# Performance work log

Hardware: AMD Instinct MI355X
Metric: run time of the kernel (lower is better)

The kernel has to match this reference:

```python
import jax, jax.numpy as jnp
import numpy as np

NUM_HEADS = 16
HEAD_DIM = 64  # hidden = 1024


def setup_inputs() -> dict:
    key = jax.random.key(0)
    k1, k2, k3 = jax.random.split(key, 3)
    B, S, Hd = 4, 4096, NUM_HEADS * HEAD_DIM
    x = jax.random.normal(k1, (B, S, Hd), dtype=jnp.float32)
    # xavier-uniform-ish scaling for the dense kernels
    Wqkv = jax.random.normal(k2, (Hd, 3 * Hd), dtype=jnp.float32) * (2.0 / (Hd + 3 * Hd)) ** 0.5
    bqkv = jnp.zeros((3 * Hd,), dtype=jnp.float32)
    Wout = jax.random.normal(k3, (Hd, Hd), dtype=jnp.float32) * (1.0 / Hd) ** 0.5
    bout = jnp.zeros((Hd,), dtype=jnp.float32)
    return {"x": x, "Wqkv": Wqkv, "bqkv": bqkv, "Wout": Wout, "bout": bout}


def reference(x, Wqkv, bqkv, Wout, bout):
    B, S, _ = x.shape
    H, D = NUM_HEADS, HEAD_DIM
    qkv = jnp.einsum('bsc,cf->bsf', x, Wqkv) + bqkv  # [B,S,3*H*D]
    q, k, v = jnp.split(qkv, 3, axis=-1)
    # source transposes to [B,H,S,D] before calling flax dot_product_attention_weights,
    # which interprets dims as [..., q_len=H, num_heads=S, depth=D]  (shape bug, kept faithfully)
    q = q.reshape(B, S, H, D).transpose(0, 2, 1, 3)  # [B,H,S,D]
    k = k.reshape(B, S, H, D).transpose(0, 2, 1, 3)
    v = v.reshape(B, S, H, D).transpose(0, 2, 1, 3)
    scale = D ** -0.5
    # flax: einsum('...qhd,...khd->...hqk') -> weights [B, S, H, H]
    logits = jnp.einsum('bqhd,bkhd->bhqk', q * scale, k)
    attn = jax.nn.softmax(logits, axis=-1)  # softmax over key-head axis
    # source: einsum('bhqk,bkhd->bqhd', weights, v) -> [B, H, S, D]
    out = jnp.einsum('bhqk,bkhd->bqhd', attn, v)
    out = out.transpose(0, 2, 1, 3).reshape(B, S, H * D)  # [B,S,hidden]
    return jnp.einsum('bsc,cf->bsf', out, Wout) + bout
```

## Files before the change

kernel.cpp:

```cpp
#include <hip/hip_runtime.h>
#include <hip/hip_bf16.h>

using bf16 = __hip_bfloat16;
typedef __bf16 bf16x8_t __attribute__((ext_vector_type(8)));
typedef float f32x4_t __attribute__((ext_vector_type(4)));

__device__ __forceinline__ void gl16(bf16* l, const bf16* g) {
  __builtin_amdgcn_global_load_lds(
      (const __attribute__((address_space(1))) unsigned int*)g,
      (__attribute__((address_space(3))) unsigned int*)l, 16, 0, 0);
}

#define BARRIER() do { asm volatile("" ::: "memory"); __builtin_amdgcn_s_barrier(); asm volatile("" ::: "memory"); } while (0)
#define WAITVM(N) asm volatile("s_waitcnt vmcnt(" #N ")" ::: "memory")
#define SCHED0() __builtin_amdgcn_sched_barrier(0)

__global__ __launch_bounds__(256) void cvt_f32_bf16(const float* __restrict__ in,
                                                    bf16* __restrict__ out, int n4) {
  int i = blockIdx.x * 256 + threadIdx.x;
  if (i >= n4) return;
  float4 v = ((const float4*)in)[i];
  union { ushort4 u; bf16 b[4]; } o;
  o.b[0] = __float2bfloat16(v.x);
  o.b[1] = __float2bfloat16(v.y);
  o.b[2] = __float2bfloat16(v.z);
  o.b[3] = __float2bfloat16(v.w);
  ((ushort4*)out)[i] = o.u;
}

__global__ __launch_bounds__(256) void transpose_cvt(const float* __restrict__ in,
                                                     bf16* __restrict__ out, int R, int C) {
  __shared__ float t[32][33];
  int bx = blockIdx.x * 32, by = blockIdx.y * 32;
  int tx = threadIdx.x & 31, ty = threadIdx.x >> 5;
#pragma unroll
  for (int r = 0; r < 32; r += 8)
    t[ty + r][tx] = in[(size_t)(by + ty + r) * C + bx + tx];
  __syncthreads();
#pragma unroll
  for (int r = 0; r < 32; r += 8)
    out[(size_t)(bx + ty + r) * R + by + tx] = __float2bfloat16(t[tx][ty + r]);
}


__device__ __forceinline__ void readA(const bf16* lb, int half, int wr, int lr, int lg, int exr,
                                      bf16x8_t (&af)[4][2]) {
  const bf16* ab = lb + half * 8192;
#pragma unroll
  for (int mi = 0; mi < 4; ++mi) {
    int R = wr * 64 + mi * 16 + lr;
    af[mi][0] = *(const bf16x8_t*)(ab + R * 64 + ((lg * 8) ^ exr));
    af[mi][1] = *(const bf16x8_t*)(ab + R * 64 + ((32 + lg * 8) ^ exr));
  }
}
__device__ __forceinline__ void readB(const bf16* lb, int half, int wc, int lr, int lg, int exr,
                                      bf16x8_t (&bfr)[2][2]) {
  const bf16* bb = lb + (2 + half) * 8192;
#pragma unroll
  for (int ni = 0; ni < 2; ++ni) {
    int R = wc * 32 + ni * 16 + lr;
    bfr[ni][0] = *(const bf16x8_t*)(bb + R * 64 + ((lg * 8) ^ exr));
    bfr[ni][1] = *(const bf16x8_t*)(bb + R * 64 + ((32 + lg * 8) ^ exr));
  }
}

template <int MH, int NH>
__device__ __forceinline__ void mfma16(bf16x8_t (&af)[4][2], bf16x8_t (&bfr)[2][2],
                                       f32x4_t (&acc)[8][4]) {
  __builtin_amdgcn_s_setprio(1);
#pragma unroll
  for (int mi = 0; mi < 4; ++mi)
#pragma unroll
    for (int ni = 0; ni < 2; ++ni) {
      f32x4_t& a = acc[MH * 4 + mi][NH * 2 + ni];
      a = __builtin_amdgcn_mfma_f32_16x16x32_bf16(af[mi][0], bfr[ni][0], a, 0, 0, 0);
      a = __builtin_amdgcn_mfma_f32_16x16x32_bf16(af[mi][1], bfr[ni][1], a, 0, 0, 0);
    }
  __builtin_amdgcn_s_setprio(0);
}

template <int OUT_BF16, int NWGX>
__global__ __launch_bounds__(512, 2) void gemm256p(const bf16* __restrict__ A,
                                                   const bf16* __restrict__ Bt,
                                                   const float* __restrict__ bias,
                                                   void* __restrict__ Cv) {
  constexpr int K = 1024;
  constexpr int N = NWGX * 256;
  constexpr int TT = NWGX / 4;
  constexpr int G = TT * 16;
  constexpr int CPX = NWGX * 8;

  __shared__ __align__(16) bf16 lds[65536];
  const int tid = threadIdx.x;
  const int bx = blockIdx.x;

  const int wid = tid >> 6, lane = tid & 63;
  const int wr = wid >> 2, wc = wid & 3;
  const int lr = lane & 15, lg = lane >> 4;
  const int exr = (lr & 7) << 3;

  const int srow = tid >> 3;
  const int colg = ((((tid & 7) * 16) ^ ((srow & 7) << 4)) >> 1);
  const int browc0 = (srow >> 5) * 64 + (srow & 31);

  auto tileMN = [&](int tt, int& m0, int& n0) {
    int orig = bx + (tt << 8);
    int swz = (orig & 7) * CPX + (orig >> 3);
    m0 = (swz / NWGX) * 256;
    n0 = (swz % NWGX) * 256;
  };

  auto stageA = [&](int g, int h) {
    if (g >= G) return;
    int m0, n0; tileMN(g >> 4, m0, n0);
    const bf16* g0 = A + (size_t)(m0 + h * 64 + srow) * K + (g & 15) * 64 + colg;
    bf16* l = lds + (g & 1) * 32768 + h * 8192 + tid * 8;
    gl16(l, g0); gl16(l + 4096, g0 + (size_t)128 * K);
  };
  auto stageB = [&](int g, int h) {
    if (g >= G) return;
    int m0, n0; tileMN(g >> 4, m0, n0);
    const bf16* g0 = Bt + (size_t)(n0 + browc0 + h * 32) * K + (g & 15) * 64 + colg;
    bf16* l = lds + (g & 1) * 32768 + (2 + h) * 8192 + tid * 8;
    gl16(l, g0); gl16(l + 4096, g0 + (size_t)128 * K);
  };

  f32x4_t acc[8][4] = {};
  bf16x8_t af1[4][2], af2[4][2], b0[2][2], b1[2][2];

  stageA(0, 0); stageB(0, 0); stageA(0, 1); stageB(0, 1);
  stageA(1, 0); stageB(1, 0);
  WAITVM(4);
  BARRIER();
  readA(lds, 0, wr, lr, lg, exr, af1);
  readB(lds, 0, wc, lr, lg, exr, b0);

  for (int g = 0; g < G; ++g) {
    const bf16* cb = lds + (g & 1) * 32768;
    const bf16* nb = lds + ((g & 1) ^ 1) * 32768;

    stageA(g + 1, 1);
    BARRIER();
    readB(cb, 1, wc, lr, lg, exr, b1);
    SCHED0();
    mfma16<0, 0>(af1, b0, acc);
    BARRIER();

    stageB(g + 1, 1);
    BARRIER();
    readA(cb, 1, wr, lr, lg, exr, af2);
    SCHED0();
    mfma16<0, 1>(af1, b1, acc);
    BARRIER();

    stageA(g + 2, 0);
    BARRIER();
    mfma16<1, 0>(af2, b0, acc);
    BARRIER();

    stageB(g + 2, 0);
    if (g < G - 2) { WAITVM(4); } else { WAITVM(0); }
    BARRIER();
    readA(nb, 0, wr, lr, lg, exr, af1);
    readB(nb, 0, wc, lr, lg, exr, b0);
    SCHED0();
    mfma16<1, 1>(af2, b1, acc);
    BARRIER();

    if ((g & 15) == 15) {
      int m0, n0; tileMN(g >> 4, m0, n0);
      float bv[4];
#pragma unroll
      for (int n = 0; n < 4; ++n) bv[n] = bias[n0 + wc * 64 + n * 16 + lr];
#pragma unroll
      for (int m = 0; m < 8; ++m) {
        int row = m0 + wr * 128 + m * 16 + lg * 4;
#pragma unroll
        for (int j = 0; j < 4; ++j) {
#pragma unroll
          for (int n = 0; n < 4; ++n) {
            int col = n0 + wc * 64 + n * 16 + lr;
            float v = acc[m][n][j] + bv[n];
            if (OUT_BF16)
              ((bf16*)Cv)[(size_t)(row + j) * N + col] = __float2bfloat16(v);
            else
              ((float*)Cv)[(size_t)(row + j) * N + col] = v;
            acc[m][n][j] = 0.f;
          }
        }
      }
    }
  }
}

#define PSTR 48
__global__ __launch_bounds__(256) void attn_tok(const bf16* __restrict__ qkv,
                                                bf16* __restrict__ out) {
  __shared__ __align__(16) bf16 vs[4][1024];
  __shared__ __align__(16) bf16 ps[4][16 * PSTR];
  const int w = threadIdx.x >> 6, l = threadIdx.x & 63;
  const int t = blockIdx.x * 4 + w;
  const int lr = l & 15, lg = l >> 4;
  const bf16* base = qkv + (size_t)t * 3072;

  bf16x8_t v0 = *(const bf16x8_t*)(base + 2048 + l * 16);
  bf16x8_t v1 = *(const bf16x8_t*)(base + 2048 + l * 16 + 8);
  *(bf16x8_t*)(&vs[w][l * 16]) = v0;
  *(bf16x8_t*)(&vs[w][l * 16 + 8]) = v1;

  *(unsigned long long*)(&ps[w][(l >> 2) * PSTR + 16 + (l & 3) * 4]) = 0ULL;

  const bf16* qp = base + lr * 64 + lg * 8;
  const bf16* kp = base + 1024 + lr * 64 + lg * 8;
  bf16x8_t qa0 = *(const bf16x8_t*)qp;
  bf16x8_t ka0 = *(const bf16x8_t*)kp;
  bf16x8_t qa1 = *(const bf16x8_t*)(qp + 32);
  bf16x8_t ka1 = *(const bf16x8_t*)(kp + 32);
  f32x4_t s = {};
  s = __builtin_amdgcn_mfma_f32_16x16x32_bf16(qa0, ka0, s, 0, 0, 0);
  s = __builtin_amdgcn_mfma_f32_16x16x32_bf16(qa1, ka1, s, 0, 0, 0);

#pragma unroll
  for (int j = 0; j < 4; ++j) {
    float x = s[j] * 0.125f;
    float mx = x;
#pragma unroll
    for (int off = 8; off; off >>= 1) mx = fmaxf(mx, __shfl_xor(mx, off, 16));
    float e = __expf(x - mx);
    float sum = e;
#pragma unroll
    for (int off = 8; off; off >>= 1) sum += __shfl_xor(sum, off, 16);
    ps[w][(lg * 4 + j) * PSTR + lr] = __float2bfloat16(e / sum);
  }

  bf16x8_t pf = *(const bf16x8_t*)(&ps[w][lr * PSTR + lg * 8]);
  bf16x8_t vf[4] = {};
  if (l < 32) {
#pragma unroll
    for (int c = 0; c < 4; ++c)
#pragma unroll
      for (int j = 0; j < 8; ++j)
        vf[c][j] = (__bf16)vs[w][(lg * 8 + j) * 64 + c * 16 + lr];
  }
  f32x4_t o[4] = {};
#pragma unroll
  for (int c = 0; c < 4; ++c)
    o[c] = __builtin_amdgcn_mfma_f32_16x16x32_bf16(pf, vf[c], o[c], 0, 0, 0);

  bf16* ob = out + (size_t)t * 1024;
#pragma unroll
  for (int c = 0; c < 4; ++c)
#pragma unroll
    for (int j = 0; j < 4; ++j)
      ob[(lg * 4 + j) * 64 + c * 16 + lr] = __float2bfloat16(o[c][j]);
}

extern "C" void kernel_launch(void* const* d_in, const int* in_sizes, int n_in,
                              void* d_out, int out_size, void* d_ws, size_t ws_size,
                              hipStream_t stream) {
  const float* x    = (const float*)d_in[0];
  const float* Wqkv = (const float*)d_in[1];
  const float* bqkv = (const float*)d_in[2];
  const float* Wout = (const float*)d_in[3];
  const float* bout = (const float*)d_in[4];
  float* y = (float*)d_out;

  const int T = 16384, HD = 1024, N1 = 3072;

  char* ws = (char*)d_ws;
  size_t off = 0;
  bf16* xb  = (bf16*)(ws + off); off += (size_t)T * HD * 2;
  bf16* w1t = (bf16*)(ws + off); off += (size_t)N1 * HD * 2;
  bf16* w2t = (bf16*)(ws + off); off += (size_t)HD * HD * 2;
  bf16* qkv = (bf16*)(ws + off); off += (size_t)T * N1 * 2;
  if (ws_size < off) return;
  bf16* ao = xb;

  cvt_f32_bf16<<<(T * HD / 4 + 255) / 256, 256, 0, stream>>>(x, xb, T * HD / 4);
  transpose_cvt<<<dim3(N1 / 32, HD / 32), 256, 0, stream>>>(Wqkv, w1t, HD, N1);
  transpose_cvt<<<dim3(HD / 32, HD / 32), 256, 0, stream>>>(Wout, w2t, HD, HD);

  gemm256p<1, 12><<<256, 512, 0, stream>>>(xb, w1t, bqkv, qkv);
  attn_tok<<<T / 4, 256, 0, stream>>>(qkv, ao);
  gemm256p<0, 4><<<256, 512, 0, stream>>>(ao, w2t, bout, y);
}
```

Measured before the change: 207.6 us.

## Restructure GEMM main loop per tile with cross-tile prefetch, merge weight transposes

The persistent GEMM loop is split into an outer per-tile loop and an inner k-step loop that uses precomputed base pointers, so address and tile-swizzle math leave the hot loop. The first k-steps of the next tile are prefetched during the tail of the current tile, which removes the per-step G bounds checks. Sched barriers and the trailing barriers after each MFMA block are dropped, and the two weight transpose launches become one. The trade-off is more complex code with unroll 2, and removing barriers risks LDS hazards and higher register pressure.

```diff
diff --git a/kernel.cpp b/kernel.cpp
--- a/kernel.cpp
+++ b/kernel.cpp
@@ -13,7 +13,31 @@
 
 #define BARRIER() do { asm volatile("" ::: "memory"); __builtin_amdgcn_s_barrier(); asm volatile("" ::: "memory"); } while (0)
 #define WAITVM(N) asm volatile("s_waitcnt vmcnt(" #N ")" ::: "memory")
-#define SCHED0() __builtin_amdgcn_sched_barrier(0)
+
+__global__ __launch_bounds__(256) void prep_t(const float* __restrict__ Wqkv,
+                                              const float* __restrict__ Wout,
+                                              bf16* __restrict__ w1t,
+                                              bf16* __restrict__ w2t) {
+  __shared__ float t[32][33];
+  const int bid = blockIdx.x;
+  const float* in; bf16* out; int R, C, gx, gy;
+  if (bid < 3072) {
+    in = Wqkv; out = w1t; R = 1024; C = 3072;
+    gx = bid % 96; gy = bid / 96;
+  } else {
+    int idx = bid - 3072; in = Wout; out = w2t; R = 1024; C = 1024;
+    gx = idx & 31; gy = idx >> 5;
+  }
+  int bx = gx * 32, by = gy * 32;
+  int tx = threadIdx.x & 31, ty = threadIdx.x >> 5;
+#pragma unroll
+  for (int r = 0; r < 32; r += 8)
+    t[ty + r][tx] = in[(size_t)(by + ty + r) * C + bx + tx];
+  __syncthreads();
+#pragma unroll
+  for (int r = 0; r < 32; r += 8)
+    out[(size_t)(bx + ty + r) * R + by + tx] = __float2bfloat16(t[tx][ty + r]);
+}
 
 __global__ __launch_bounds__(256) void cvt_f32_bf16(const float* __restrict__ in,
                                                     bf16* __restrict__ out, int n4) {
@@ -28,21 +52,6 @@
   ((ushort4*)out)[i] = o.u;
 }
 
-__global__ __launch_bounds__(256) void transpose_cvt(const float* __restrict__ in,
-                                                     bf16* __restrict__ out, int R, int C) {
-  __shared__ float t[32][33];
-  int bx = blockIdx.x * 32, by = blockIdx.y * 32;
-  int tx = threadIdx.x & 31, ty = threadIdx.x >> 5;
-#pragma unroll
-  for (int r = 0; r < 32; r += 8)
-    t[ty + r][tx] = in[(size_t)(by + ty + r) * C + bx + tx];
-  __syncthreads();
-#pragma unroll
-  for (int r = 0; r < 32; r += 8)
-    out[(size_t)(bx + ty + r) * R + by + tx] = __float2bfloat16(t[tx][ty + r]);
-}
-
-
 __device__ __forceinline__ void readA(const bf16* lb, int half, int wr, int lr, int lg, int exr,
                                       bf16x8_t (&af)[4][2]) {
   const bf16* ab = lb + half * 8192;
@@ -87,7 +96,6 @@
   constexpr int K = 1024;
   constexpr int N = NWGX * 256;
   constexpr int TT = NWGX / 4;
-  constexpr int G = TT * 16;
   constexpr int CPX = NWGX * 8;
 
   __shared__ __align__(16) bf16 lds[65536];
@@ -110,65 +118,118 @@
     n0 = (swz % NWGX) * 256;
   };
 
-  auto stageA = [&](int g, int h) {
-    if (g >= G) return;
-    int m0, n0; tileMN(g >> 4, m0, n0);
-    const bf16* g0 = A + (size_t)(m0 + h * 64 + srow) * K + (g & 15) * 64 + colg;
-    bf16* l = lds + (g & 1) * 32768 + h * 8192 + tid * 8;
+  bf16* const ldsSt = lds + tid * 8;
+  auto stA = [&](const bf16* pA, int s, int h, int par) {
+    const bf16* g0 = pA + h * 65536 + s * 64;
+    bf16* l = ldsSt + par * 32768 + h * 8192;
     gl16(l, g0); gl16(l + 4096, g0 + (size_t)128 * K);
   };
-  auto stageB = [&](int g, int h) {
-    if (g >= G) return;
-    int m0, n0; tileMN(g >> 4, m0, n0);
-    const bf16* g0 = Bt + (size_t)(n0 + browc0 + h * 32) * K + (g & 15) * 64 + colg;
-    bf16* l = lds + (g & 1) * 32768 + (2 + h) * 8192 + tid * 8;
+  auto stB = [&](const bf16* pB, int s, int h, int par) {
+    const bf16* g0 = pB + h * 32768 + s * 64;
+    bf16* l = ldsSt + par * 32768 + (2 + h) * 8192;
     gl16(l, g0); gl16(l + 4096, g0 + (size_t)128 * K);
   };
 
   f32x4_t acc[8][4] = {};
   bf16x8_t af1[4][2], af2[4][2], b0[2][2], b1[2][2];
 
-  stageA(0, 0); stageB(0, 0); stageA(0, 1); stageB(0, 1);
-  stageA(1, 0); stageB(1, 0);
+  int m0, n0;
+  tileMN(0, m0, n0);
+  const bf16* pA = A + (size_t)(m0 + srow) * K + colg;
+  const bf16* pB = Bt + (size_t)(n0 + browc0) * K + colg;
+
+  stA(pA, 0, 0, 0); stB(pB, 0, 0, 0); stA(pA, 0, 1, 0); stB(pB, 0, 1, 0);
+  stA(pA, 1, 0, 1); stB(pB, 1, 0, 1);
   WAITVM(4);
   BARRIER();
   readA(lds, 0, wr, lr, lg, exr, af1);
   readB(lds, 0, wc, lr, lg, exr, b0);
 
-  for (int g = 0; g < G; ++g) {
-    const bf16* cb = lds + (g & 1) * 32768;
-    const bf16* nb = lds + ((g & 1) ^ 1) * 32768;
-
-    stageA(g + 1, 1);
+  for (int tt = 0; tt < TT; ++tt) {
+    const bool last = (tt == TT - 1);
+    int m0x, n0x;
+    tileMN(last ? tt : tt + 1, m0x, n0x);
+    const bf16* pAn = A + (size_t)(m0x + srow) * K + colg;
+    const bf16* pBn = Bt + (size_t)(n0x + browc0) * K + colg;
+
+#pragma unroll 2
+    for (int s = 0; s < 14; ++s) {
+      const int par = s & 1, parn = par ^ 1;
+      const bf16* cb = lds + par * 32768;
+      const bf16* nb = lds + parn * 32768;
+
+      stA(pA, s + 1, 1, parn);
+      BARRIER();
+      readB(cb, 1, wc, lr, lg, exr, b1);
+      mfma16<0, 0>(af1, b0, acc);
+
+      stB(pB, s + 1, 1, parn);
+      BARRIER();
+      readA(cb, 1, wr, lr, lg, exr, af2);
+      mfma16<0, 1>(af1, b1, acc);
+
+      stA(pA, s + 2, 0, par);
+      BARRIER();
+      mfma16<1, 0>(af2, b0, acc);
+
+      stB(pB, s + 2, 0, par);
+      WAITVM(4);
+      BARRIER();
+      readA(nb, 0, wr, lr, lg, exr, af1);
+      readB(nb, 0, wc, lr, lg, exr, b0);
+      mfma16<1, 1>(af2, b1, acc);
+    }
+    {
+      const bf16* cb = lds;
+      const bf16* nb = lds + 32768;
+      stA(pA, 15, 1, 1);
+      BARRIER();
+      readB(cb, 1, wc, lr, lg, exr, b1);
+      mfma16<0, 0>(af1, b0, acc);
+
+      stB(pB, 15, 1, 1);
+      BARRIER();
+      readA(cb, 1, wr, lr, lg, exr, af2);
+      mfma16<0, 1>(af1, b1, acc);
+
+      if (!last) stA(pAn, 0, 0, 0);
+      BARRIER();
+      mfma16<1, 0>(af2, b0, acc);
+
+      if (!last) { stB(pBn, 0, 0, 0); WAITVM(4); } else { WAITVM(0); }
+      BARRIER();
+      readA(nb, 0, wr, lr, lg, exr, af1);
+      readB(nb, 0, wc, lr, lg, exr, b0);
+      mfma16<1, 1>(af2, b1, acc);
+    }
+    {
+      const bf16* cb = lds + 32768;
+      const bf16* nb = lds;
+      if (!last) stA(pAn, 0, 1, 0);
+      BARRIER();
+      readB(cb, 1, wc, lr, lg, exr, b1);
+      mfma16<0, 0>(af1, b0, acc);
+
+      if (!last) stB(pBn, 0, 1, 0);
+      BARRIER();
+      readA(cb, 1, wr, lr, lg, exr, af2);
+      mfma16<0, 1>(af1, b1, acc);
+
+      if (!last) stA(pAn, 1, 0, 1);
+      BARRIER();
+      mfma16<1, 0>(af2, b0, acc);
+
+      if (!last) { stB(pBn, 1, 0, 1); WAITVM(4); }
+      BARRIER();
+      if (!last) {
+        readA(nb, 0, wr, lr, lg, exr, af1);
+        readB(nb, 0, wc, lr, lg, exr, b0);
+      }
+      mfma16<1, 1>(af2, b1, acc);
+    }
+
     BARRIER();
-    readB(cb, 1, wc, lr, lg, exr, b1);
-    SCHED0();
-    mfma16<0, 0>(af1, b0, acc);
-    BARRIER();
-
-    stageB(g + 1, 1);
-    BARRIER();
-    readA(cb, 1, wr, lr, lg, exr, af2);
-    SCHED0();
-    mfma16<0, 1>(af1, b1, acc);
-    BARRIER();
-
-    stageA(g + 2, 0);
-    BARRIER();
-    mfma16<1, 0>(af2, b0, acc);
-    BARRIER();
-
-    stageB(g + 2, 0);
-    if (g < G - 2) { WAITVM(4); } else { WAITVM(0); }
-    BARRIER();
-    readA(nb, 0, wr, lr, lg, exr, af1);
-    readB(nb, 0, wc, lr, lg, exr, b0);
-    SCHED0();
-    mfma16<1, 1>(af2, b1, acc);
-    BARRIER();
-
-    if ((g & 15) == 15) {
-      int m0, n0; tileMN(g >> 4, m0, n0);
+    {
       float bv[4];
 #pragma unroll
       for (int n = 0; n < 4; ++n) bv[n] = bias[n0 + wc * 64 + n * 16 + lr];
@@ -190,6 +251,7 @@
         }
       }
     }
+    pA = pAn; pB = pBn; m0 = m0x; n0 = n0x;
   }
 }
 
@@ -276,10 +338,8 @@
   if (ws_size < off) return;
   bf16* ao = xb;
 
-  cvt_f32_bf16<<<(T * HD / 4 + 255) / 256, 256, 0, stream>>>(x, xb, T * HD / 4);
-  transpose_cvt<<<dim3(N1 / 32, HD / 32), 256, 0, stream>>>(Wqkv, w1t, HD, N1);
-  transpose_cvt<<<dim3(HD / 32, HD / 32), 256, 0, stream>>>(Wout, w2t, HD, HD);
-
+  cvt_f32_bf16<<<T * HD / 4 / 256, 256, 0, stream>>>(x, xb, T * HD / 4);
+  prep_t<<<3072 + 1024, 256, 0, stream>>>(Wqkv, Wout, w1t, w2t);
   gemm256p<1, 12><<<256, 512, 0, stream>>>(xb, w1t, bqkv, qkv);
   attn_tok<<<T / 4, 256, 0, stream>>>(qkv, ao);
   gemm256p<0, 4><<<256, 512, 0, stream>>>(ao, w2t, bout, y);
```

After: 263.2 us. +26.8%, slower.
